# Performance work log

Hardware: AMD Instinct MI355X
Metric: run time of the kernel (lower is better)

## Reference

```python
import jax, jax.numpy as jnp
import numpy as np
from functools import partial

MODES = 16384
WIDTH = 2048
ALPHA = 0.5
B, C, H, W = 1, 1, 128, 128
BN_EPS = 1e-5


def _conv2d(x, w, b):
    # x: NCHW, w: OIHW, 3x3 SAME padding, stride 1
    y = jax.lax.conv_general_dilated(x, w, (1, 1), 'SAME',
                                     dimension_numbers=('NCHW', 'OIHW', 'NCHW'))
    return y + b[None, :, None, None]


def _bn(x, g, b):
    # BatchNorm2d in training mode: batch statistics over (N,H,W), biased var
    m = x.mean(axis=(0, 2, 3), keepdims=True)
    v = x.var(axis=(0, 2, 3), keepdims=True)
    return (x - m) * jax.lax.rsqrt(v + BN_EPS) * g[None, :, None, None] + b[None, :, None, None]


def _lin(x, w, b):
    # torch Linear convention: w is (out, in)
    return x @ w.T + b


def _gl_fractional(xf, alpha):
    # Grunwald-Letnikov fractional derivative on a 1D signal sampled on t=linspace(0,1,n):
    #   D^a f(t_k) ~= h^{-a} * sum_{j=0}^{k} w_j f(t_{k-j}),  w_0=1, w_j = w_{j-1}*(j-1-a)/j
    # Implemented as an FFT-based causal convolution.
    n = xf.shape[0]
    h = 1.0 / (n - 1)
    j = jnp.arange(1, n, dtype=xf.dtype)
    gl_w = jnp.concatenate([jnp.ones((1,), xf.dtype), jnp.cumprod((j - 1.0 - alpha) / j)])
    L = 2 * n  # power of two here (n=16384)
    y = jnp.fft.irfft(jnp.fft.rfft(xf, L) * jnp.fft.rfft(gl_w, L), L)[:n]
    return y * (h ** (-alpha))


def setup_inputs() -> dict:
    key = jax.random.key(0)
    ks = jax.random.split(key, 24)

    def lin_p(k, out_d, in_d):
        k1, k2 = jax.random.split(k)
        s = 1.0 / np.sqrt(in_d)
        return (jax.random.uniform(k1, (out_d, in_d), jnp.float32, -s, s),
                jax.random.uniform(k2, (out_d,), jnp.float32, -s, s))

    def conv_p(k, out_c, in_c):
        k1, k2 = jax.random.split(k)
        s = 1.0 / np.sqrt(in_c * 9)
        return (jax.random.uniform(k1, (out_c, in_c, 3, 3), jnp.float32, -s, s),
                jax.random.uniform(k2, (out_c,), jnp.float32, -s, s))

    conv1_w, conv1_b = conv_p(ks[0], 16, 1)
    conv2_w, conv2_b = conv_p(ks[1], 32, 16)
    conv3_w, conv3_b = conv_p(ks[2], 1, 32)
    enc_w1, enc_b1 = lin_p(ks[3], WIDTH, MODES)
    enc_w2, enc_b2 = lin_p(ks[4], WIDTH, WIDTH)
    enc_w3, enc_b3 = lin_p(ks[5], MODES, WIDTH)
    op_w1, op_b1 = lin_p(ks[6], WIDTH, MODES)
    op_w2, op_b2 = lin_p(ks[7], WIDTH, WIDTH)
    op_w3, op_b3 = lin_p(ks[8], MODES, WIDTH)

    return {
        'x': jax.random.normal(ks[9], (B, C, H, W), jnp.float32),
        'conv1_w': conv1_w, 'conv1_b': conv1_b,
        'bn1_g': jnp.ones((16,), jnp.float32), 'bn1_b': jnp.zeros((16,), jnp.float32),
        'conv2_w': conv2_w, 'conv2_b': conv2_b,
        'bn2_g': jnp.ones((32,), jnp.float32), 'bn2_b': jnp.zeros((32,), jnp.float32),
        'conv3_w': conv3_w, 'conv3_b': conv3_b,
        'enc_w1': enc_w1, 'enc_b1': enc_b1, 'enc_w2': enc_w2, 'enc_b2': enc_b2,
        'enc_w3': enc_w3, 'enc_b3': enc_b3,
        'op_w1': op_w1, 'op_b1': op_b1, 'op_w2': op_w2, 'op_b2': op_b2,
        'op_w3': op_w3, 'op_b3': op_b3,
    }


def reference(x, conv1_w, conv1_b, bn1_g, bn1_b, conv2_w, conv2_b, bn2_g, bn2_b,
              conv3_w, conv3_b, enc_w1, enc_b1, enc_w2, enc_b2, enc_w3, enc_b3,
              op_w1, op_b1, op_w2, op_b2, op_w3, op_b3):
    bsz = x.shape[0]
    total = x.size

    # Conv / BN / ReLU encoder stack
    xc = jax.nn.relu(_bn(_conv2d(x, conv1_w, conv1_b), bn1_g, bn1_b))
    xc = jax.nn.relu(_bn(_conv2d(xc, conv2_w, conv2_b), bn2_g, bn2_b))
    xc = _conv2d(xc, conv3_w, conv3_b)

    # flatten and keep first `modes` features
    x_flat = xc.reshape(bsz, -1)[:, :MODES]

    # MLP encoder (modes -> width -> width -> modes)
    x_frac = _lin(jax.nn.relu(_lin(jax.nn.relu(_lin(x_flat, enc_w1, enc_b1)), enc_w2, enc_b2)), enc_w3, enc_b3)

    # fractional operator applied to the fully-flattened tensor (as in the original)
    shp = x_frac.shape
    x_proc = _gl_fractional(x_frac.reshape(-1), ALPHA).reshape(shp)

    # neural operator MLP (modes -> width -> width -> modes)
    out_flat = _lin(jax.nn.relu(_lin(jax.nn.relu(_lin(x_proc, op_w1, op_b1)), op_w2, op_b2)), op_w3, op_b3)

    # pad/truncate bookkeeping (static shapes -> Python control flow is fine under jit)
    if out_flat.shape[-1] < total:
        out_flat = jnp.pad(out_flat, ((0, 0), (0, total - out_flat.shape[-1])))
    elif out_flat.shape[-1] > total:
        out_flat = out_flat[..., :total]
    if out_flat.size != total:
        out_flat = out_flat.reshape(-1)[:total].reshape(bsz, -1)
    return out_flat.reshape(x.shape)
```

## Files before the change

kernel.cpp:

```cpp
#include <hip/hip_runtime.h>
#include <math.h>

#define NPIX 16384
#define BN_EPS 1e-5f

__device__ __forceinline__ float wave_reduce(float v) {
#pragma unroll
    for (int off = 32; off; off >>= 1) v += __shfl_down(v, off);
    return v;
}

__global__ void k_conv1(const float* __restrict__ x, const float* __restrict__ w,
                        const float* __restrict__ b, float* __restrict__ c1,
                        float* __restrict__ stats) {
    __shared__ float xs[4][132];
    __shared__ float rs[4][16], rq[4][16];
    int t = threadIdx.x;
    int r0 = blockIdx.x * 2;
#pragma unroll
    for (int r = 0; r < 4; ++r) {
        if (t < 130) {
            int gr = r0 - 1 + r, gc = t - 1;
            float v = 0.f;
            if (gr >= 0 && gr < 128 && gc >= 0 && gc < 128) v = x[gr * 128 + gc];
            xs[r][t] = v;
        }
    }
    __syncthreads();

    int pyl = t >> 7, px = t & 127;
    int p = r0 * 128 + t;
    float nv[9];
#pragma unroll
    for (int ky = 0; ky < 3; ++ky)
#pragma unroll
        for (int kx = 0; kx < 3; ++kx) nv[ky * 3 + kx] = xs[pyl + ky][px + kx];

    int wid = t >> 6, lane = t & 63;
#pragma unroll
    for (int c = 0; c < 16; ++c) {
        float acc = b[c];
#pragma unroll
        for (int k = 0; k < 9; ++k) acc = fmaf(w[c * 9 + k], nv[k], acc);
        c1[c * NPIX + p] = acc;
        float s = wave_reduce(acc);
        float q = wave_reduce(acc * acc);
        if (lane == 0) { rs[wid][c] = s; rq[wid][c] = q; }
    }
    __syncthreads();
    if (t < 16)
        atomicAdd(&stats[t], rs[0][t] + rs[1][t] + rs[2][t] + rs[3][t]);
    else if (t < 32)
        atomicAdd(&stats[t], rq[0][t - 16] + rq[1][t - 16] + rq[2][t - 16] + rq[3][t - 16]);
}

__global__ void k_conv2(const float* __restrict__ c1, const float* __restrict__ stats1,
                        const float* __restrict__ g1, const float* __restrict__ bb1,
                        const float* __restrict__ w2, const float* __restrict__ b2,
                        float* __restrict__ c2, float* __restrict__ stats2) {
    __shared__ float xs[16][4][132];
    __shared__ float rs[4][16], rq[4][16];
    int t = threadIdx.x;
    int cg = blockIdx.x & 1;
    int chunk = blockIdx.x >> 1;
    int r0 = chunk * 2;

    for (int ch = 0; ch < 16; ++ch) {
        float m = stats1[ch] * (1.f / 16384.f);
        float v = stats1[16 + ch] * (1.f / 16384.f) - m * m;
        float s = g1[ch] * rsqrtf(v + BN_EPS);
        float sh = bb1[ch] - m * s;
#pragma unroll
        for (int r = 0; r < 4; ++r) {
            if (t < 130) {
                int gr = r0 - 1 + r, gc = t - 1;
                float val = 0.f;
                if (gr >= 0 && gr < 128 && gc >= 0 && gc < 128)
                    val = fmaxf(fmaf(c1[ch * NPIX + gr * 128 + gc], s, sh), 0.f);
                xs[ch][r][t] = val;
            }
        }
    }
    __syncthreads();

    int pyl = t >> 7, px = t & 127;
    int p = r0 * 128 + t;
    float acc[16];
#pragma unroll
    for (int o = 0; o < 16; ++o) acc[o] = b2[cg * 16 + o];

    for (int ch = 0; ch < 16; ++ch) {
        float nv[9];
#pragma unroll
        for (int ky = 0; ky < 3; ++ky)
#pragma unroll
            for (int kx = 0; kx < 3; ++kx) nv[ky * 3 + kx] = xs[ch][pyl + ky][px + kx];
#pragma unroll
        for (int o = 0; o < 16; ++o) {
            int oc = cg * 16 + o;
#pragma unroll
            for (int k = 0; k < 9; ++k)
                acc[o] = fmaf(w2[oc * 144 + ch * 9 + k], nv[k], acc[o]);
        }
    }

    int wid = t >> 6, lane = t & 63;
#pragma unroll
    for (int o = 0; o < 16; ++o) {
        int oc = cg * 16 + o;
        c2[oc * NPIX + p] = acc[o];
        float s = wave_reduce(acc[o]);
        float q = wave_reduce(acc[o] * acc[o]);
        if (lane == 0) { rs[wid][o] = s; rq[wid][o] = q; }
    }
    __syncthreads();
    if (t < 16)
        atomicAdd(&stats2[cg * 16 + t], rs[0][t] + rs[1][t] + rs[2][t] + rs[3][t]);
    else if (t < 32)
        atomicAdd(&stats2[32 + cg * 16 + (t - 16)],
                  rq[0][t - 16] + rq[1][t - 16] + rq[2][t - 16] + rq[3][t - 16]);
}

__global__ void k_conv3(const float* __restrict__ c2, const float* __restrict__ stats2,
                        const float* __restrict__ g2, const float* __restrict__ bb2,
                        const float* __restrict__ w3, const float* __restrict__ b3,
                        float* __restrict__ xflat) {
    __shared__ float xs[32][3][132];
    int t = threadIdx.x;
    int row = blockIdx.x;

    for (int ch = 0; ch < 32; ++ch) {
        float m = stats2[ch] * (1.f / 16384.f);
        float v = stats2[32 + ch] * (1.f / 16384.f) - m * m;
        float s = g2[ch] * rsqrtf(v + BN_EPS);
        float sh = bb2[ch] - m * s;
#pragma unroll
        for (int r = 0; r < 3; ++r) {
            if (t < 130) {
                int gr = row - 1 + r, gc = t - 1;
                float val = 0.f;
                if (gr >= 0 && gr < 128 && gc >= 0 && gc < 128)
                    val = fmaxf(fmaf(c2[ch * NPIX + gr * 128 + gc], s, sh), 0.f);
                xs[ch][r][t] = val;
            }
        }
    }
    __syncthreads();

    if (t < 128) {
        float acc = b3[0];
        for (int ch = 0; ch < 32; ++ch) {
#pragma unroll
            for (int ky = 0; ky < 3; ++ky)
#pragma unroll
                for (int kx = 0; kx < 3; ++kx)
                    acc = fmaf(w3[ch * 9 + ky * 3 + kx], xs[ch][ky][t + kx], acc);
        }
        xflat[row * 128 + t] = acc;
    }
}

__global__ void k_glw(float* __restrict__ glw) {
    int j = blockIdx.x * 256 + threadIdx.x;
    double scale = sqrt(16383.0);
    double wj;
    if (j == 0)
        wj = 1.0;
    else
        wj = -exp(lgamma((double)j - 0.5) - lgamma((double)j + 1.0)) / 3.5449077018110318;
    glw[j] = (float)(wj * scale);
}

__global__ void k_glconv(const float* __restrict__ glw, const float* __restrict__ x,
                         float* __restrict__ y) {
    __shared__ float w_s[256];
    __shared__ float x_s[511];
    int bid = blockIdx.x;
    int bi = (int)((sqrtf(8.f * (float)bid + 1.f) - 1.f) * 0.5f);
    while ((bi + 1) * (bi + 2) / 2 <= bid) ++bi;
    while (bi * (bi + 1) / 2 > bid) --bi;
    int bj = bid - bi * (bi + 1) / 2;

    int ti = threadIdx.x;
    w_s[ti] = glw[256 * bj + ti];
    int xbase = 256 * (bi - bj) - 255;
#pragma unroll
    for (int k = ti; k < 511; k += 256) {
        int g = xbase + k;
        x_s[k] = (g >= 0) ? x[g] : 0.f;
    }
    __syncthreads();

    float p = 0.f;
#pragma unroll 8
    for (int jj = 0; jj < 256; ++jj)
        p = fmaf(w_s[jj], x_s[ti - jj + 255], p);

    atomicAdd(&y[256 * bi + ti], p);
}

template <int N, bool RELU>
__global__ void gemv_block(const float* __restrict__ Wm, const float* __restrict__ bias,
                           const float* __restrict__ x, float* __restrict__ y) {
    int row = blockIdx.x;
    const float4* Wr = reinterpret_cast<const float4*>(Wm + (size_t)row * N);
    const float4* xv = reinterpret_cast<const float4*>(x);
    constexpr int N4 = N >> 2;
    float acc = 0.f;
#pragma unroll 4
    for (int i = threadIdx.x; i < N4; i += 256) {
        float4 a = Wr[i];
        float4 b = xv[i];
        acc = fmaf(a.x, b.x, acc);
        acc = fmaf(a.y, b.y, acc);
        acc = fmaf(a.z, b.z, acc);
        acc = fmaf(a.w, b.w, acc);
    }
    __shared__ float red[4];
    float s = wave_reduce(acc);
    int wid = threadIdx.x >> 6, lane = threadIdx.x & 63;
    if (lane == 0) red[wid] = s;
    __syncthreads();
    if (threadIdx.x == 0) {
        float t = red[0] + red[1] + red[2] + red[3] + bias[row];
        if (RELU) t = fmaxf(t, 0.f);
        y[row] = t;
    }
}

template <int N, bool RELU>
__global__ void gemv_wave(const float* __restrict__ Wm, const float* __restrict__ bias,
                          const float* __restrict__ x, float* __restrict__ y) {
    int wid = threadIdx.x >> 6, lane = threadIdx.x & 63;
    int row = blockIdx.x * 4 + wid;
    const float4* Wr = reinterpret_cast<const float4*>(Wm + (size_t)row * N);
    const float4* xv = reinterpret_cast<const float4*>(x);
    constexpr int N4 = N >> 2;
    float acc = 0.f;
#pragma unroll 4
    for (int i = lane; i < N4; i += 64) {
        float4 a = Wr[i];
        float4 b = xv[i];
        acc = fmaf(a.x, b.x, acc);
        acc = fmaf(a.y, b.y, acc);
        acc = fmaf(a.z, b.z, acc);
        acc = fmaf(a.w, b.w, acc);
    }
    float s = wave_reduce(acc);
    if (lane == 0) {
        float t = s + bias[row];
        if (RELU) t = fmaxf(t, 0.f);
        y[row] = t;
    }
}

extern "C" void kernel_launch(void* const* d_in, const int* in_sizes, int n_in,
                              void* d_out, int out_size, void* d_ws, size_t ws_size,
                              hipStream_t stream) {
    const float* x       = (const float*)d_in[0];
    const float* conv1_w = (const float*)d_in[1];
    const float* conv1_b = (const float*)d_in[2];
    const float* bn1_g   = (const float*)d_in[3];
    const float* bn1_b   = (const float*)d_in[4];
    const float* conv2_w = (const float*)d_in[5];
    const float* conv2_b = (const float*)d_in[6];
    const float* bn2_g   = (const float*)d_in[7];
    const float* bn2_b   = (const float*)d_in[8];
    const float* conv3_w = (const float*)d_in[9];
    const float* conv3_b = (const float*)d_in[10];
    const float* enc_w1  = (const float*)d_in[11];
    const float* enc_b1  = (const float*)d_in[12];
    const float* enc_w2  = (const float*)d_in[13];
    const float* enc_b2  = (const float*)d_in[14];
    const float* enc_w3  = (const float*)d_in[15];
    const float* enc_b3  = (const float*)d_in[16];
    const float* op_w1   = (const float*)d_in[17];
    const float* op_b1   = (const float*)d_in[18];
    const float* op_w2   = (const float*)d_in[19];
    const float* op_b2   = (const float*)d_in[20];
    const float* op_w3   = (const float*)d_in[21];
    const float* op_b3   = (const float*)d_in[22];
    float* out = (float*)d_out;

    float* ws = (float*)d_ws;
    float* c1    = ws;
    float* c2    = ws + 262144;
    float* xflat = ws + 786432;
    float* y1    = ws + 802816;
    float* y2    = ws + 804864;
    float* xfrac = ws + 806912;
    float* glw   = ws + 823296;
    float* z1    = ws + 839680;
    float* z2    = ws + 841728;
    float* xproc = ws + 843776;
    float* stats = ws + 860160;

    hipMemsetAsync(xproc, 0, (16384 + 96) * sizeof(float), stream);

    k_glw<<<64, 256, 0, stream>>>(glw);

    k_conv1<<<64, 256, 0, stream>>>(x, conv1_w, conv1_b, c1, stats);
    k_conv2<<<128, 256, 0, stream>>>(c1, stats, bn1_g, bn1_b, conv2_w, conv2_b,
                                     c2, stats + 32);
    k_conv3<<<128, 256, 0, stream>>>(c2, stats + 32, bn2_g, bn2_b, conv3_w, conv3_b,
                                     xflat);

    gemv_block<16384, true><<<2048, 256, 0, stream>>>(enc_w1, enc_b1, xflat, y1);
    gemv_wave<2048, true><<<512, 256, 0, stream>>>(enc_w2, enc_b2, y1, y2);
    gemv_wave<2048, false><<<4096, 256, 0, stream>>>(enc_w3, enc_b3, y2, xfrac);

    k_glconv<<<2080, 256, 0, stream>>>(glw, xfrac, xproc);

    gemv_block<16384, true><<<2048, 256, 0, stream>>>(op_w1, op_b1, xproc, z1);
    gemv_wave<2048, true><<<512, 256, 0, stream>>>(op_w2, op_b2, z1, z2);
    gemv_wave<2048, false><<<4096, 256, 0, stream>>>(op_w3, op_b3, z2, out);
}
```

Baseline: 603.3 us.

## Split conv channel groups, fold memset into glw kernel, two-row GEMV waves

Several changes land together. The memset is folded into the GL-weight kernel, which now zeroes xflat, xproc and stats. conv2 and conv3 are split over more blocks by channel group, with conv3 accumulating partial sums through atomics, and their shared-memory fills become strided cooperative loops. The 2048-wide GEMVs process two rows per wave so each x load is reused. The aim is to cut launch overhead and raise parallelism in the small conv stages, but the total is likely dominated by memory-bound weight streaming, which these changes barely affect.

```diff
diff --git a/kernel.cpp b/kernel.cpp
--- a/kernel.cpp
+++ b/kernel.cpp
@@ -8,6 +8,19 @@
 #pragma unroll
     for (int off = 32; off; off >>= 1) v += __shfl_down(v, off);
     return v;
+}
+
+__global__ void k_glw(float* __restrict__ glw, float* __restrict__ zr) {
+    int j = blockIdx.x * 256 + threadIdx.x;
+    zr[j] = 0.f;
+    zr[16384 + j] = 0.f;
+    if (j < 96) zr[32768 + j] = 0.f;
+    double wj;
+    if (j == 0)
+        wj = 1.0;
+    else
+        wj = -exp(lgamma((double)j - 0.5) - lgamma((double)j + 1.0)) / 3.5449077018110318;
+    glw[j] = (float)(wj * sqrt(16383.0));
 }
 
 __global__ void k_conv1(const float* __restrict__ x, const float* __restrict__ w,
@@ -17,14 +30,12 @@
     __shared__ float rs[4][16], rq[4][16];
     int t = threadIdx.x;
     int r0 = blockIdx.x * 2;
-#pragma unroll
-    for (int r = 0; r < 4; ++r) {
-        if (t < 130) {
-            int gr = r0 - 1 + r, gc = t - 1;
-            float v = 0.f;
-            if (gr >= 0 && gr < 128 && gc >= 0 && gc < 128) v = x[gr * 128 + gc];
-            xs[r][t] = v;
-        }
+    for (int idx = t; idx < 4 * 132; idx += 256) {
+        int r = idx / 132, c = idx - r * 132;
+        int gr = r0 - 1 + r, gc = c - 1;
+        float v = 0.f;
+        if (c < 130 && gr >= 0 && gr < 128 && gc >= 0 && gc < 128) v = x[gr * 128 + gc];
+        xs[r][c] = v;
     }
     __syncthreads();
 
@@ -59,35 +70,39 @@
                         const float* __restrict__ w2, const float* __restrict__ b2,
                         float* __restrict__ c2, float* __restrict__ stats2) {
     __shared__ float xs[16][4][132];
-    __shared__ float rs[4][16], rq[4][16];
+    __shared__ float scs[16], shs[16];
+    __shared__ float rs[4][8], rq[4][8];
     int t = threadIdx.x;
-    int cg = blockIdx.x & 1;
-    int chunk = blockIdx.x >> 1;
+    int cg = blockIdx.x & 3;
+    int chunk = blockIdx.x >> 2;
     int r0 = chunk * 2;
 
-    for (int ch = 0; ch < 16; ++ch) {
-        float m = stats1[ch] * (1.f / 16384.f);
-        float v = stats1[16 + ch] * (1.f / 16384.f) - m * m;
-        float s = g1[ch] * rsqrtf(v + BN_EPS);
-        float sh = bb1[ch] - m * s;
-#pragma unroll
-        for (int r = 0; r < 4; ++r) {
-            if (t < 130) {
-                int gr = r0 - 1 + r, gc = t - 1;
-                float val = 0.f;
-                if (gr >= 0 && gr < 128 && gc >= 0 && gc < 128)
-                    val = fmaxf(fmaf(c1[ch * NPIX + gr * 128 + gc], s, sh), 0.f);
-                xs[ch][r][t] = val;
-            }
-        }
+    if (t < 16) {
+        float m = stats1[t] * (1.f / 16384.f);
+        float v = stats1[16 + t] * (1.f / 16384.f) - m * m;
+        float s = g1[t] * rsqrtf(v + BN_EPS);
+        scs[t] = s;
+        shs[t] = bb1[t] - m * s;
+    }
+    __syncthreads();
+
+    for (int idx = t; idx < 16 * 4 * 132; idx += 256) {
+        int ch = idx / 528;
+        int rem = idx - ch * 528;
+        int r = rem / 132, c = rem - r * 132;
+        int gr = r0 - 1 + r, gc = c - 1;
+        float val = 0.f;
+        if (c < 130 && gr >= 0 && gr < 128 && gc >= 0 && gc < 128)
+            val = fmaxf(fmaf(c1[ch * NPIX + gr * 128 + gc], scs[ch], shs[ch]), 0.f);
+        xs[ch][r][c] = val;
     }
     __syncthreads();
 
     int pyl = t >> 7, px = t & 127;
     int p = r0 * 128 + t;
-    float acc[16];
-#pragma unroll
-    for (int o = 0; o < 16; ++o) acc[o] = b2[cg * 16 + o];
+    float acc[8];
+#pragma unroll
+    for (int o = 0; o < 8; ++o) acc[o] = b2[cg * 8 + o];
 
     for (int ch = 0; ch < 16; ++ch) {
         float nv[9];
@@ -96,8 +111,8 @@
 #pragma unroll
             for (int kx = 0; kx < 3; ++kx) nv[ky * 3 + kx] = xs[ch][pyl + ky][px + kx];
 #pragma unroll
-        for (int o = 0; o < 16; ++o) {
-            int oc = cg * 16 + o;
+        for (int o = 0; o < 8; ++o) {
+            int oc = cg * 8 + o;
 #pragma unroll
             for (int k = 0; k < 9; ++k)
                 acc[o] = fmaf(w2[oc * 144 + ch * 9 + k], nv[k], acc[o]);
@@ -106,69 +121,65 @@
 
     int wid = t >> 6, lane = t & 63;
 #pragma unroll
-    for (int o = 0; o < 16; ++o) {
-        int oc = cg * 16 + o;
+    for (int o = 0; o < 8; ++o) {
+        int oc = cg * 8 + o;
         c2[oc * NPIX + p] = acc[o];
         float s = wave_reduce(acc[o]);
         float q = wave_reduce(acc[o] * acc[o]);
         if (lane == 0) { rs[wid][o] = s; rq[wid][o] = q; }
     }
     __syncthreads();
-    if (t < 16)
-        atomicAdd(&stats2[cg * 16 + t], rs[0][t] + rs[1][t] + rs[2][t] + rs[3][t]);
-    else if (t < 32)
-        atomicAdd(&stats2[32 + cg * 16 + (t - 16)],
-                  rq[0][t - 16] + rq[1][t - 16] + rq[2][t - 16] + rq[3][t - 16]);
+    if (t < 8)
+        atomicAdd(&stats2[cg * 8 + t], rs[0][t] + rs[1][t] + rs[2][t] + rs[3][t]);
+    else if (t < 16)
+        atomicAdd(&stats2[32 + cg * 8 + (t - 8)],
+                  rq[0][t - 8] + rq[1][t - 8] + rq[2][t - 8] + rq[3][t - 8]);
 }
 
 __global__ void k_conv3(const float* __restrict__ c2, const float* __restrict__ stats2,
                         const float* __restrict__ g2, const float* __restrict__ bb2,
                         const float* __restrict__ w3, const float* __restrict__ b3,
                         float* __restrict__ xflat) {
-    __shared__ float xs[32][3][132];
+    __shared__ float xs[16][3][132];
+    __shared__ float scs[16], shs[16];
     int t = threadIdx.x;
-    int row = blockIdx.x;
-
-    for (int ch = 0; ch < 32; ++ch) {
+    int cg = blockIdx.x & 1;
+    int row = blockIdx.x >> 1;
+    int cb = cg * 16;
+
+    if (t < 16) {
+        int ch = cb + t;
         float m = stats2[ch] * (1.f / 16384.f);
         float v = stats2[32 + ch] * (1.f / 16384.f) - m * m;
         float s = g2[ch] * rsqrtf(v + BN_EPS);
-        float sh = bb2[ch] - m * s;
-#pragma unroll
-        for (int r = 0; r < 3; ++r) {
-            if (t < 130) {
-                int gr = row - 1 + r, gc = t - 1;
-                float val = 0.f;
-                if (gr >= 0 && gr < 128 && gc >= 0 && gc < 128)
-                    val = fmaxf(fmaf(c2[ch * NPIX + gr * 128 + gc], s, sh), 0.f);
-                xs[ch][r][t] = val;
-            }
+        scs[t] = s;
+        shs[t] = bb2[ch] - m * s;
+    }
+    __syncthreads();
+
+    for (int idx = t; idx < 16 * 3 * 132; idx += 256) {
+        int ch = idx / 396;
+        int rem = idx - ch * 396;
+        int r = rem / 132, c = rem - r * 132;
+        int gr = row - 1 + r, gc = c - 1;
+        float val = 0.f;
+        if (c < 130 && gr >= 0 && gr < 128 && gc >= 0 && gc < 128)
+            val = fmaxf(fmaf(c2[(cb + ch) * NPIX + gr * 128 + gc], scs[ch], shs[ch]), 0.f);
+        xs[ch][r][c] = val;
+    }
+    __syncthreads();
+
+    if (t < 128) {
+        float acc = (cg == 0) ? b3[0] : 0.f;
+        for (int ch = 0; ch < 16; ++ch) {
+#pragma unroll
+            for (int ky = 0; ky < 3; ++ky)
+#pragma unroll
+                for (int kx = 0; kx < 3; ++kx)
+                    acc = fmaf(w3[(cb + ch) * 9 + ky * 3 + kx], xs[ch][ky][t + kx], acc);
         }
-    }
-    __syncthreads();
-
-    if (t < 128) {
-        float acc = b3[0];
-        for (int ch = 0; ch < 32; ++ch) {
-#pragma unroll
-            for (int ky = 0; ky < 3; ++ky)
-#pragma unroll
-                for (int kx = 0; kx < 3; ++kx)
-                    acc = fmaf(w3[ch * 9 + ky * 3 + kx], xs[ch][ky][t + kx], acc);
-        }
-        xflat[row * 128 + t] = acc;
-    }
-}
-
-__global__ void k_glw(float* __restrict__ glw) {
-    int j = blockIdx.x * 256 + threadIdx.x;
-    double scale = sqrt(16383.0);
-    double wj;
-    if (j == 0)
-        wj = 1.0;
-    else
-        wj = -exp(lgamma((double)j - 0.5) - lgamma((double)j + 1.0)) / 3.5449077018110318;
-    glw[j] = (float)(wj * scale);
+        atomicAdd(&xflat[row * 128 + t], acc);
+    }
 }
 
 __global__ void k_glconv(const float* __restrict__ glw, const float* __restrict__ x,
@@ -199,16 +210,15 @@
     atomicAdd(&y[256 * bi + ti], p);
 }
 
-template <int N, bool RELU>
+template <bool RELU>
 __global__ void gemv_block(const float* __restrict__ Wm, const float* __restrict__ bias,
                            const float* __restrict__ x, float* __restrict__ y) {
     int row = blockIdx.x;
-    const float4* Wr = reinterpret_cast<const float4*>(Wm + (size_t)row * N);
+    const float4* Wr = reinterpret_cast<const float4*>(Wm + (size_t)row * 16384);
     const float4* xv = reinterpret_cast<const float4*>(x);
-    constexpr int N4 = N >> 2;
     float acc = 0.f;
 #pragma unroll 4
-    for (int i = threadIdx.x; i < N4; i += 256) {
+    for (int i = threadIdx.x; i < 4096; i += 256) {
         float4 a = Wr[i];
         float4 b = xv[i];
         acc = fmaf(a.x, b.x, acc);
@@ -228,29 +238,33 @@
     }
 }
 
-template <int N, bool RELU>
-__global__ void gemv_wave(const float* __restrict__ Wm, const float* __restrict__ bias,
-                          const float* __restrict__ x, float* __restrict__ y) {
+template <bool RELU>
+__global__ void gemv2(const float* __restrict__ Wm, const float* __restrict__ bias,
+                      const float* __restrict__ x, float* __restrict__ y) {
     int wid = threadIdx.x >> 6, lane = threadIdx.x & 63;
-    int row = blockIdx.x * 4 + wid;
-    const float4* Wr = reinterpret_cast<const float4*>(Wm + (size_t)row * N);
+    int r0 = (blockIdx.x * 4 + wid) * 2;
+    const float4* W0 = reinterpret_cast<const float4*>(Wm + (size_t)r0 * 2048);
+    const float4* W1 = reinterpret_cast<const float4*>(Wm + (size_t)(r0 + 1) * 2048);
     const float4* xv = reinterpret_cast<const float4*>(x);
-    constexpr int N4 = N >> 2;
-    float acc = 0.f;
-#pragma unroll 4
-    for (int i = lane; i < N4; i += 64) {
-        float4 a = Wr[i];
+    float a0 = 0.f, a1 = 0.f;
+#pragma unroll
+    for (int i = lane; i < 512; i += 64) {
         float4 b = xv[i];
-        acc = fmaf(a.x, b.x, acc);
-        acc = fmaf(a.y, b.y, acc);
-        acc = fmaf(a.z, b.z, acc);
-        acc = fmaf(a.w, b.w, acc);
-    }
-    float s = wave_reduce(acc);
+        float4 u = W0[i];
+        float4 v = W1[i];
+        a0 = fmaf(u.x, b.x, a0); a0 = fmaf(u.y, b.y, a0);
+        a0 = fmaf(u.z, b.z, a0); a0 = fmaf(u.w, b.w, a0);
+        a1 = fmaf(v.x, b.x, a1); a1 = fmaf(v.y, b.y, a1);
+        a1 = fmaf(v.z, b.z, a1); a1 = fmaf(v.w, b.w, a1);
+    }
+    a0 = wave_reduce(a0);
+    a1 = wave_reduce(a1);
     if (lane == 0) {
-        float t = s + bias[row];
-        if (RELU) t = fmaxf(t, 0.f);
-        y[row] = t;
+        float t0 = a0 + bias[r0];
+        float t1 = a1 + bias[r0 + 1];
+        if (RELU) { t0 = fmaxf(t0, 0.f); t1 = fmaxf(t1, 0.f); }
+        y[r0] = t0;
+        y[r0 + 1] = t1;
     }
 }
 
@@ -283,35 +297,33 @@
     float* out = (float*)d_out;
 
     float* ws = (float*)d_ws;
-    float* c1    = ws;
-    float* c2    = ws + 262144;
-    float* xflat = ws + 786432;
-    float* y1    = ws + 802816;
-    float* y2    = ws + 804864;
-    float* xfrac = ws + 806912;
-    float* glw   = ws + 823296;
-    float* z1    = ws + 839680;
-    float* z2    = ws + 841728;
-    float* xproc = ws + 843776;
-    float* stats = ws + 860160;
-
-    hipMemsetAsync(xproc, 0, (16384 + 96) * sizeof(float), stream);
-
-    k_glw<<<64, 256, 0, stream>>>(glw);
+    float* xflat = ws;
+    float* xproc = ws + 16384;
+    float* stats = ws + 32768;
+    float* glw   = ws + 32960;
+    float* c1    = ws + 49344;
+    float* c2    = ws + 311488;
+    float* y1    = ws + 835776;
+    float* y2    = ws + 837824;
+    float* xfrac = ws + 839872;
+    float* z1    = ws + 856256;
+    float* z2    = ws + 858304;
+
+    k_glw<<<64, 256, 0, stream>>>(glw, ws);
 
     k_conv1<<<64, 256, 0, stream>>>(x, conv1_w, conv1_b, c1, stats);
-    k_conv2<<<128, 256, 0, stream>>>(c1, stats, bn1_g, bn1_b, conv2_w, conv2_b,
+    k_conv2<<<256, 256, 0, stream>>>(c1, stats, bn1_g, bn1_b, conv2_w, conv2_b,
                                      c2, stats + 32);
-    k_conv3<<<128, 256, 0, stream>>>(c2, stats + 32, bn2_g, bn2_b, conv3_w, conv3_b,
+    k_conv3<<<256, 256, 0, stream>>>(c2, stats + 32, bn2_g, bn2_b, conv3_w, conv3_b,
                                      xflat);
 
-    gemv_block<16384, true><<<2048, 256, 0, stream>>>(enc_w1, enc_b1, xflat, y1);
-    gemv_wave<2048, true><<<512, 256, 0, stream>>>(enc_w2, enc_b2, y1, y2);
-    gemv_wave<2048, false><<<4096, 256, 0, stream>>>(enc_w3, enc_b3, y2, xfrac);
+    gemv_block<true><<<2048, 256, 0, stream>>>(enc_w1, enc_b1, xflat, y1);
+    gemv2<true><<<256, 256, 0, stream>>>(enc_w2, enc_b2, y1, y2);
+    gemv2<false><<<2048, 256, 0, stream>>>(enc_w3, enc_b3, y2, xfrac);
 
     k_glconv<<<2080, 256, 0, stream>>>(glw, xfrac, xproc);
 
-    gemv_block<16384, true><<<2048, 256, 0, stream>>>(op_w1, op_b1, xproc, z1);
-    gemv_wave<2048, true><<<512, 256, 0, stream>>>(op_w2, op_b2, z1, z2);
-    gemv_wave<2048, false><<<4096, 256, 0, stream>>>(op_w3, op_b3, z2, out);
-}
+    gemv_block<true><<<2048, 256, 0, stream>>>(op_w1, op_b1, xproc, z1);
+    gemv2<true><<<256, 256, 0, stream>>>(op_w2, op_b2, z1, z2);
+    gemv2<false><<<2048, 256, 0, stream>>>(op_w3, op_b3, z2, out);
+}
```

New measurement: 552.4 us. 1.09x faster.
